# Kernel tuning notes

Measured on AMD Instinct MI355X. Metric: run time of the kernel, lower is better.

The kernel has to match this reference:

```python
import jax, jax.numpy as jnp
import numpy as np

HIDDEN = 4096
N_HEADS = 32
N_KV_HEADS = 8
HEAD_DIM = HIDDEN // N_HEADS  # 128
ROPE_THETA = 10000.0


def rotate_half(x):
    x1, x2 = jnp.split(x, 2, axis=-1)
    return jnp.concatenate((-x2, x1), axis=-1)


def rope_cos_sin(seq_len, dim, theta, dtype):
    inv_freq = 1.0 / (theta ** (jnp.arange(0, dim, 2, dtype=jnp.float32) / dim))
    t = jnp.arange(seq_len, dtype=jnp.float32)
    freqs = jnp.outer(t, inv_freq)               # [S, D/2]
    emb = jnp.concatenate((freqs, freqs), axis=-1)  # [S, D]
    return jnp.cos(emb).astype(dtype), jnp.sin(emb).astype(dtype)


def setup_inputs() -> dict:
    key = jax.random.key(0)
    k0, k1, k2, k3, k4 = jax.random.split(key, 5)
    B, S = 1, 2048
    std = 1.0 / np.sqrt(HIDDEN)
    return {
        "hidden_states": jax.random.normal(k0, (B, S, HIDDEN), dtype=jnp.float32),
        "wq": jax.random.normal(k1, (N_HEADS * HEAD_DIM, HIDDEN), dtype=jnp.float32) * std,
        "wk": jax.random.normal(k2, (N_KV_HEADS * HEAD_DIM, HIDDEN), dtype=jnp.float32) * std,
        "wv": jax.random.normal(k3, (N_KV_HEADS * HEAD_DIM, HIDDEN), dtype=jnp.float32) * std,
        "wo": jax.random.normal(k4, (HIDDEN, N_HEADS * HEAD_DIM), dtype=jnp.float32) * std,
    }


def reference(hidden_states, wq, wk, wv, wo):
    B, S, _ = hidden_states.shape
    dtype = hidden_states.dtype
    G = N_HEADS // N_KV_HEADS  # query groups per kv head

    # projections (torch Linear: x @ W.T)
    q = (hidden_states @ wq.T).reshape(B, S, N_HEADS, HEAD_DIM).transpose(0, 2, 1, 3)      # [B,H,S,D]
    k = (hidden_states @ wk.T).reshape(B, S, N_KV_HEADS, HEAD_DIM).transpose(0, 2, 1, 3)   # [B,Hkv,S,D]
    v = (hidden_states @ wv.T).reshape(B, S, N_KV_HEADS, HEAD_DIM).transpose(0, 2, 1, 3)   # [B,Hkv,S,D]

    cos, sin = rope_cos_sin(S, HEAD_DIM, ROPE_THETA, dtype)  # [S,D]
    cos = cos[None, None]  # [1,1,S,D]
    sin = sin[None, None]
    q = q * cos + rotate_half(q) * sin
    k = k * cos + rotate_half(k) * sin

    # GQA: group query heads with their kv head (equivalent to repeat_interleave on kv)
    qg = q.reshape(B, N_KV_HEADS, G, S, HEAD_DIM)
    scale = 1.0 / np.sqrt(HEAD_DIM)
    scores = jnp.einsum("bkgsd,bktd->bkgst", qg, k) * scale  # [B,Hkv,G,S,S]

    causal = jnp.tril(jnp.ones((S, S), dtype=bool))
    scores = jnp.where(causal, scores, -jnp.inf)
    probs = jax.nn.softmax(scores.astype(jnp.float32), axis=-1).astype(dtype)

    out = jnp.einsum("bkgst,bktd->bkgsd", probs, v)  # [B,Hkv,G,S,D]
    out = out.reshape(B, N_HEADS, S, HEAD_DIM).transpose(0, 2, 1, 3).reshape(B, S, N_HEADS * HEAD_DIM)
    return out @ wo.T
```

## Files before the change

kernel.cpp:

```cpp
#include <hip/hip_runtime.h>
#include <hip/hip_bf16.h>


typedef _Float16 half4_t __attribute__((ext_vector_type(4)));
typedef _Float16 half8_t __attribute__((ext_vector_type(8)));
typedef float f32x4 __attribute__((ext_vector_type(4)));

#define S_LEN 2048
#define HID 4096
#define NH 32
#define NKV 8

__device__ __forceinline__ void gload_lds16(const void* g, void* l) {
  __builtin_amdgcn_global_load_lds((const __attribute__((address_space(1))) void*)g,
                                   (__attribute__((address_space(3))) void*)l, 16, 0, 0);
}

__global__ __launch_bounds__(256) void cvt_f32_f16(const float* __restrict__ src,
                                                   _Float16* __restrict__ dst, int n4) {
  int i = blockIdx.x * 256 + threadIdx.x;
  if (i >= n4) return;
  f32x4 v = *(const f32x4*)(src + (size_t)i * 4);
  half4_t h = {(_Float16)v[0], (_Float16)v[1], (_Float16)v[2], (_Float16)v[3]};
  *(half4_t*)(dst + (size_t)i * 4) = h;
}

__global__ __launch_bounds__(256) void rope_table_kernel(float* __restrict__ cost,
                                                         float* __restrict__ sint) {
  int i = blockIdx.x * 256 + threadIdx.x;
  int d = i & 63;
  int s = i >> 6;
  float inv = exp2f(-(float)d * (13.287712379549449f / 64.0f));
  float f = (float)s * inv;
  cost[i] = cosf(f);
  sint[i] = sinf(f);
}

__global__ __launch_bounds__(256) void rope_apply_q(_Float16* __restrict__ X,
                                                    const float* __restrict__ cost,
                                                    const float* __restrict__ sint) {
  int idx = blockIdx.x * 256 + threadIdx.x;
  int g = idx & 15;
  int tmp = idx >> 4;
  int h = tmp % NH;
  int s = tmp / NH;
  int d0 = g * 4;
  size_t base = (size_t)s * HID + h * 128 + d0;
  half4_t x1 = *(half4_t*)(X + base);
  half4_t x2 = *(half4_t*)(X + base + 64);
  const float* cp = cost + s * 64 + d0;
  const float* sp = sint + s * 64 + d0;
  half4_t y1, y2;
#pragma unroll
  for (int j = 0; j < 4; ++j) {
    float c = cp[j], sn = sp[j];
    float a = (float)x1[j], b = (float)x2[j];
    y1[j] = (_Float16)(a * c - b * sn);
    y2[j] = (_Float16)(b * c + a * sn);
  }
  *(half4_t*)(X + base) = y1;
  *(half4_t*)(X + base + 64) = y2;
}

__global__ __launch_bounds__(256) void rope_k2_inplace(_Float16* __restrict__ K2,
                                                       const float* __restrict__ cost,
                                                       const float* __restrict__ sint) {
  int idx = blockIdx.x * 256 + threadIdx.x;
  int g = idx & 15;
  int tmp = idx >> 4;
  int h = tmp % NKV;
  int s = tmp / NKV;
  int d0 = g * 4;
  size_t tb = (size_t)h * (S_LEN * 128) + (size_t)(s >> 4) * 2048 + (size_t)(s & 15) * 8;
  size_t a1 = tb + (size_t)(d0 >> 3) * 128 + (d0 & 7);
  size_t a2 = a1 + 1024;
  half4_t x1 = *(half4_t*)(K2 + a1);
  half4_t x2 = *(half4_t*)(K2 + a2);
  const float* cp = cost + s * 64 + d0;
  const float* sp = sint + s * 64 + d0;
  half4_t y1, y2;
#pragma unroll
  for (int j = 0; j < 4; ++j) {
    float c = cp[j], sn = sp[j];
    float a = (float)x1[j], b = (float)x2[j];
    y1[j] = (_Float16)(a * c - b * sn);
    y2[j] = (_Float16)(b * c + a * sn);
  }
  *(half4_t*)(K2 + a1) = y1;
  *(half4_t*)(K2 + a2) = y2;
}

template <int MODE>
__global__ __launch_bounds__(256) void gemm5(const _Float16* __restrict__ A,
                                             const _Float16* __restrict__ W0,
                                             const _Float16* __restrict__ W1,
                                             const _Float16* __restrict__ W2,
                                             void* __restrict__ out,
                                             _Float16* __restrict__ K2,
                                             _Float16* __restrict__ V2, int bxoff) {
  __shared__ __align__(16) _Float16 As[2][128 * 32];
  __shared__ __align__(16) _Float16 Bs[2][128 * 32];
  const int t = threadIdx.x, w = t >> 6, l = t & 63, lr = l & 15, lg = l >> 4;
  const int nwg = gridDim.x * gridDim.y;
  const int flat = blockIdx.y * gridDim.x + blockIdx.x;
  const int rm = (flat & 7) * (nwg >> 3) + (flat >> 3);
  const int bx = rm % gridDim.x + bxoff;
  const int by = rm / gridDim.x;
  const int m0 = by * 128;
  const _Float16* Wsel;
  int col0, sel;
  if (MODE == 1) {
    Wsel = W0; col0 = bx * 128; sel = 0;
  } else {
    if (bx < 32)      { Wsel = W0; col0 = bx * 128; sel = 0; }
    else if (bx < 40) { Wsel = W1; col0 = (bx - 32) * 128; sel = 1; }
    else              { Wsel = W2; col0 = (bx - 40) * 128; sel = 2; }
  }
  const int wm = (w >> 1) * 64, wn = (w & 1) * 64;
  const int srow = l >> 2, scol = (l & 3) * 8;
  const _Float16* ap = A + (size_t)m0 * 4096 + scol;
  const _Float16* bp = Wsel + (size_t)col0 * 4096 + scol;
  f32x4 acc[4][4] = {};

#define STAGE5(as_, bs_, kb_)                                     \
  _Pragma("unroll") for (int it = 0; it < 2; ++it) {              \
    const int ci = it * 4 + w;                                    \
    const int r = ci * 16 + srow;                                 \
    gload_lds16(ap + (size_t)r * 4096 + (kb_), (as_) + ci * 512); \
    gload_lds16(bp + (size_t)r * 4096 + (kb_), (bs_) + ci * 512); \
  }

  STAGE5(As[0], Bs[0], 0)
  __syncthreads();
  int cur = 0;
  for (int kb = 0; kb < 4096; kb += 32) {
    if (kb + 32 < 4096) {
      STAGE5(As[cur ^ 1], Bs[cur ^ 1], kb + 32)
    }
    half8_t af[4], bf[4];
#pragma unroll
    for (int mi = 0; mi < 4; ++mi)
      af[mi] = *(const half8_t*)(As[cur] + (wm + mi * 16 + lr) * 32 + lg * 8);
#pragma unroll
    for (int ni = 0; ni < 4; ++ni)
      bf[ni] = *(const half8_t*)(Bs[cur] + (wn + ni * 16 + lr) * 32 + lg * 8);
#pragma unroll
    for (int mi = 0; mi < 4; ++mi)
#pragma unroll
      for (int ni = 0; ni < 4; ++ni)
        acc[mi][ni] = __builtin_amdgcn_mfma_f32_16x16x32_f16(af[mi], bf[ni], acc[mi][ni], 0, 0, 0);
    __syncthreads();
    cur ^= 1;
  }
#undef STAGE5

#pragma unroll
  for (int mi = 0; mi < 4; ++mi) {
#pragma unroll
    for (int ni = 0; ni < 4; ++ni) {
      const int row = m0 + wm + mi * 16 + lg * 4;
      const int col = col0 + wn + ni * 16 + lr;
      if (MODE == 1) {
#pragma unroll
        for (int i = 0; i < 4; ++i)
          ((float*)out)[(size_t)(row + i) * 4096 + col] = acc[mi][ni][i];
      } else if (sel == 0) {
#pragma unroll
        for (int i = 0; i < 4; ++i)
          ((_Float16*)out)[(size_t)(row + i) * 4096 + col] = (_Float16)acc[mi][ni][i];
      } else if (sel == 1) {
        const int h = col >> 7, d = col & 127;
        const size_t kb2 = (size_t)h * (S_LEN * 128) + (size_t)(row >> 4) * 2048 +
                           (size_t)(d >> 3) * 128 + (d & 7);
#pragma unroll
        for (int i = 0; i < 4; ++i)
          K2[kb2 + ((row + i) & 15) * 8] = (_Float16)acc[mi][ni][i];
      } else {
        half4_t o;
#pragma unroll
        for (int i = 0; i < 4; ++i) o[i] = (_Float16)acc[mi][ni][i];
        *(half4_t*)(V2 + (size_t)(col >> 7) * (S_LEN * 128) + (size_t)(row >> 4) * 2048 +
                    (size_t)(col & 127) * 16 + (row & 15)) = o;
      }
    }
  }
}

__global__ __launch_bounds__(256) void attn_kernel(const _Float16* __restrict__ Q,
                                                   const _Float16* __restrict__ K2,
                                                   const _Float16* __restrict__ V2,
                                                   _Float16* __restrict__ Op,
                                                   float* __restrict__ Md) {
  const int bid = blockIdx.x;
  const int hk = bid & 7;
  const int split = (bid >> 3) & 1;
  const int qt = 63 - (bid >> 4);
  const int w = threadIdx.x >> 6;
  const int h = hk * 4 + w;
  const int l = threadIdx.x & 63;
  const int lr = l & 15;
  const int lg = l >> 4;
  const float scale = 0.08838834764831845f;
  const float LOG2E = 1.4426950408889634f;
  const float NEG = -1.0e30f;

  const int half_steps = qt + 1;
  const int kt0 = split * half_steps;
  const int kt1 = kt0 + half_steps;

  int sq[2];
  half8_t qf[2][4];
#pragma unroll
  for (int qc = 0; qc < 2; ++qc) {
    sq[qc] = qt * 32 + qc * 16 + lr;
#pragma unroll
    for (int c = 0; c < 4; ++c)
      qf[qc][c] = *(const half8_t*)(Q + (size_t)sq[qc] * HID + h * 128 + c * 32 + lg * 8);
  }
  const _Float16* Kb = K2 + (size_t)hk * (S_LEN * 128);
  const _Float16* Vb = V2 + (size_t)hk * (S_LEN * 128);

  f32x4 acc[8][2] = {};
  float m[2] = {NEG, NEG};
  float den[2] = {0.f, 0.f};

  for (int kt = kt0; kt < kt1; ++kt) {
    half8_t kf[4];
#pragma unroll
    for (int c = 0; c < 4; ++c)
      kf[c] = *(const half8_t*)(Kb + (size_t)kt * 2048 + (c * 4 + lg) * 128 + lr * 8);
    f32x4 s0 = {0.f, 0.f, 0.f, 0.f}, s1 = {0.f, 0.f, 0.f, 0.f};
#pragma unroll
    for (int c = 0; c < 4; ++c) {
      s0 = __builtin_amdgcn_mfma_f32_16x16x32_f16(kf[c], qf[0][c], s0, 0, 0, 0);
      s1 = __builtin_amdgcn_mfma_f32_16x16x32_f16(kf[c], qf[1][c], s1, 0, 0, 0);
    }
    const int kbase = kt * 16 + lg * 4;
    float sc[2][4];
#pragma unroll
    for (int i = 0; i < 4; ++i) {
      sc[0][i] = s0[i] * scale;
      sc[1][i] = s1[i] * scale;
    }
    if (kt >= 2 * qt) {
#pragma unroll
      for (int qc = 0; qc < 2; ++qc)
#pragma unroll
        for (int i = 0; i < 4; ++i)
          if (kbase + i > sq[qc]) sc[qc][i] = NEG;
    }
    half4_t pf[2];
#pragma unroll
    for (int qc = 0; qc < 2; ++qc) {
      float mx = fmaxf(fmaxf(sc[qc][0], sc[qc][1]), fmaxf(sc[qc][2], sc[qc][3]));
      mx = fmaxf(mx, __shfl_xor(mx, 16));
      mx = fmaxf(mx, __shfl_xor(mx, 32));
      if (!__all(mx - m[qc] <= 8.0f)) {
        float mn = fmaxf(m[qc], mx);
        float corr = exp2f((m[qc] - mn) * LOG2E);
        den[qc] *= corr;
#pragma unroll
        for (int dc = 0; dc < 8; ++dc)
#pragma unroll
          for (int i = 0; i < 4; ++i) acc[dc][qc][i] *= corr;
        m[qc] = mn;
      }
      float ps = 0.f, p[4];
#pragma unroll
      for (int i = 0; i < 4; ++i) {
        p[i] = exp2f((sc[qc][i] - m[qc]) * LOG2E);
        ps += p[i];
      }
      ps += __shfl_xor(ps, 16);
      ps += __shfl_xor(ps, 32);
      den[qc] += ps;
      pf[qc] = (half4_t){(_Float16)p[0], (_Float16)p[1], (_Float16)p[2], (_Float16)p[3]};
    }
#pragma unroll
    for (int dc = 0; dc < 8; ++dc) {
      half4_t vf = *(const half4_t*)(Vb + (size_t)kt * 2048 + (dc * 16 + lr) * 16 + lg * 4);
      acc[dc][0] = __builtin_amdgcn_mfma_f32_16x16x16f16(vf, pf[0], acc[dc][0], 0, 0, 0);
      acc[dc][1] = __builtin_amdgcn_mfma_f32_16x16x16f16(vf, pf[1], acc[dc][1], 0, 0, 0);
    }
  }

  _Float16* Os = Op + (size_t)split * S_LEN * HID;
#pragma unroll
  for (int qc = 0; qc < 2; ++qc) {
    float inv = den[qc] > 0.f ? 1.0f / den[qc] : 0.f;
#pragma unroll
    for (int dc = 0; dc < 8; ++dc) {
      half4_t o;
#pragma unroll
      for (int i = 0; i < 4; ++i) o[i] = (_Float16)(acc[dc][qc][i] * inv);
      *(half4_t*)(Os + (size_t)sq[qc] * HID + h * 128 + dc * 16 + lg * 4) = o;
    }
    if (lg == 0) {
      int mdix = ((split * S_LEN + sq[qc]) * NH + h) * 2;
      Md[mdix] = m[qc];
      Md[mdix + 1] = den[qc];
    }
  }
}

__global__ __launch_bounds__(256) void attn_combine(const _Float16* __restrict__ Op,
                                                    const float* __restrict__ Md,
                                                    _Float16* __restrict__ O) {
  const float LOG2E = 1.4426950408889634f;
  int idx = blockIdx.x * 256 + threadIdx.x;
  int dd = (idx & 15) * 8;
  int h = (idx >> 4) & 31;
  int s = idx >> 9;
  int base = (s * NH + h) * 2;
  float m0 = Md[base], den0 = Md[base + 1];
  float m1 = Md[S_LEN * NH * 2 + base], den1 = Md[S_LEN * NH * 2 + base + 1];
  float M = fmaxf(m0, m1);
  float w0 = den0 * exp2f((m0 - M) * LOG2E);
  float w1 = den1 * exp2f((m1 - M) * LOG2E);
  float r = 1.0f / (w0 + w1);
  w0 *= r;
  w1 *= r;
  size_t off = (size_t)s * HID + h * 128 + dd;
  half8_t a = *(const half8_t*)(Op + off);
  half8_t b = *(const half8_t*)(Op + (size_t)S_LEN * HID + off);
  half8_t o;
#pragma unroll
  for (int j = 0; j < 8; ++j) o[j] = (_Float16)(w0 * (float)a[j] + w1 * (float)b[j]);
  *(half8_t*)(O + off) = o;
}

extern "C" void kernel_launch(void* const* d_in, const int* in_sizes, int n_in,
                              void* d_out, int out_size, void* d_ws, size_t ws_size,
                              hipStream_t stream) {
  (void)in_sizes; (void)n_in; (void)out_size;
  const float* hs = (const float*)d_in[0];
  const float* wq = (const float*)d_in[1];
  const float* wk = (const float*)d_in[2];
  const float* wv = (const float*)d_in[3];
  const float* wo = (const float*)d_in[4];

  char* ws = (char*)d_ws;
  _Float16* hs_h = (_Float16*)(ws);
  _Float16* K2   = (_Float16*)(ws + (32u << 20));
  _Float16* V2   = (_Float16*)(ws + (36u << 20));
  float* cost    = (float*)(ws + (40u << 20));
  float* sint    = (float*)(ws + (40u << 20) + (512u << 10));
  _Float16* q_h  = (_Float16*)(ws + (16u << 20));
  _Float16* wbuf = (_Float16*)(ws + (41u << 20));
  _Float16* Op   = wbuf;
  float* Md      = (float*)(ws + (73u << 20));
  _Float16* o_h  = hs_h;

  cvt_f32_f16<<<8192, 256, 0, stream>>>(hs, hs_h, (S_LEN * HID) / 4);
  rope_table_kernel<<<(S_LEN * 64) / 256, 256, 0, stream>>>(cost, sint);

  const bool merged = ws_size >= (90ull << 20);
  if (merged) {
    _Float16* wk_h = (_Float16*)(ws + (73u << 20));
    _Float16* wv_h = (_Float16*)(ws + (81u << 20));
    cvt_f32_f16<<<16384, 256, 0, stream>>>(wq, wbuf, (HID * HID) / 4);
    cvt_f32_f16<<<4096, 256, 0, stream>>>(wk, wk_h, (NKV * 128 * HID) / 4);
    cvt_f32_f16<<<4096, 256, 0, stream>>>(wv, wv_h, (NKV * 128 * HID) / 4);
    gemm5<0><<<dim3(48, 16), 256, 0, stream>>>(hs_h, wbuf, wk_h, wv_h, q_h, K2, V2, 0);
  } else {
    _Float16* wk_h = wbuf;
    _Float16* wv_h = wbuf + (8u << 20) / 2;
    cvt_f32_f16<<<16384, 256, 0, stream>>>(wq, wbuf, (HID * HID) / 4);
    gemm5<0><<<dim3(32, 16), 256, 0, stream>>>(hs_h, wbuf, nullptr, nullptr, q_h, K2, V2, 0);
    cvt_f32_f16<<<4096, 256, 0, stream>>>(wk, wk_h, (NKV * 128 * HID) / 4);
    cvt_f32_f16<<<4096, 256, 0, stream>>>(wv, wv_h, (NKV * 128 * HID) / 4);
    gemm5<0><<<dim3(16, 16), 256, 0, stream>>>(hs_h, nullptr, wk_h, wv_h, q_h, K2, V2, 32);
  }

  rope_apply_q<<<(S_LEN * NH * 16) / 256, 256, 0, stream>>>(q_h, cost, sint);
  rope_k2_inplace<<<(S_LEN * NKV * 16) / 256, 256, 0, stream>>>(K2, cost, sint);

  attn_kernel<<<1024, 256, 0, stream>>>(q_h, K2, V2, Op, Md);
  attn_combine<<<4096, 256, 0, stream>>>(Op, Md, o_h);

  cvt_f32_f16<<<16384, 256, 0, stream>>>(wo, wbuf, (HID * HID) / 4);
  gemm5<1><<<dim3(32, 16), 256, 0, stream>>>(o_h, wbuf, nullptr, nullptr, d_out, nullptr, nullptr, 0);
}
```

Baseline: 402.1 us.

## Replace GEMM with 256x256 tile ping-pong kernel and fused QKV weight conversion

Introduces a 512-thread GEMM with 256x256 output tiles, K-step 64, XOR-swizzled LDS staging, and interleaved LDS loads and MFMA phases separated by barriers with s_setprio. The Q/K/V weights are converted into one contiguous fp16 buffer by a single kernel, so one GEMM launch covers all three projections. The goal is higher data reuse and MFMA utilisation per CU and fewer launches. The trade-off is much smaller grids (192 and 128 blocks), which may leave CUs idle, and the workspace size check is removed.

```diff
diff --git a/kernel.cpp b/kernel.cpp
--- a/kernel.cpp
+++ b/kernel.cpp
@@ -23,6 +23,23 @@
   f32x4 v = *(const f32x4*)(src + (size_t)i * 4);
   half4_t h = {(_Float16)v[0], (_Float16)v[1], (_Float16)v[2], (_Float16)v[3]};
   *(half4_t*)(dst + (size_t)i * 4) = h;
+}
+
+__global__ __launch_bounds__(256) void cvt_qkv(const float* __restrict__ wq,
+                                               const float* __restrict__ wk,
+                                               const float* __restrict__ wv,
+                                               _Float16* __restrict__ dst, int n4) {
+  int i = blockIdx.x * 256 + threadIdx.x;
+  if (i >= n4) return;
+  size_t e = (size_t)i * 4;
+  const float* src;
+  size_t off;
+  if (e < (size_t)4096 * 4096)      { src = wq; off = e; }
+  else if (e < (size_t)5120 * 4096) { src = wk; off = e - (size_t)4096 * 4096; }
+  else                              { src = wv; off = e - (size_t)5120 * 4096; }
+  f32x4 v = *(const f32x4*)(src + off);
+  half4_t h = {(_Float16)v[0], (_Float16)v[1], (_Float16)v[2], (_Float16)v[3]};
+  *(half4_t*)(dst + e) = h;
 }
 
 __global__ __launch_bounds__(256) void rope_table_kernel(float* __restrict__ cost,
@@ -91,96 +108,147 @@
 }
 
 template <int MODE>
-__global__ __launch_bounds__(256) void gemm5(const _Float16* __restrict__ A,
-                                             const _Float16* __restrict__ W0,
-                                             const _Float16* __restrict__ W1,
-                                             const _Float16* __restrict__ W2,
-                                             void* __restrict__ out,
-                                             _Float16* __restrict__ K2,
-                                             _Float16* __restrict__ V2, int bxoff) {
-  __shared__ __align__(16) _Float16 As[2][128 * 32];
-  __shared__ __align__(16) _Float16 Bs[2][128 * 32];
-  const int t = threadIdx.x, w = t >> 6, l = t & 63, lr = l & 15, lg = l >> 4;
-  const int nwg = gridDim.x * gridDim.y;
-  const int flat = blockIdx.y * gridDim.x + blockIdx.x;
-  const int rm = (flat & 7) * (nwg >> 3) + (flat >> 3);
-  const int bx = rm % gridDim.x + bxoff;
-  const int by = rm / gridDim.x;
-  const int m0 = by * 128;
-  const _Float16* Wsel;
-  int col0, sel;
-  if (MODE == 1) {
-    Wsel = W0; col0 = bx * 128; sel = 0;
-  } else {
-    if (bx < 32)      { Wsel = W0; col0 = bx * 128; sel = 0; }
-    else if (bx < 40) { Wsel = W1; col0 = (bx - 32) * 128; sel = 1; }
-    else              { Wsel = W2; col0 = (bx - 40) * 128; sel = 2; }
-  }
-  const int wm = (w >> 1) * 64, wn = (w & 1) * 64;
-  const int srow = l >> 2, scol = (l & 3) * 8;
-  const _Float16* ap = A + (size_t)m0 * 4096 + scol;
-  const _Float16* bp = Wsel + (size_t)col0 * 4096 + scol;
-  f32x4 acc[4][4] = {};
-
-#define STAGE5(as_, bs_, kb_)                                     \
-  _Pragma("unroll") for (int it = 0; it < 2; ++it) {              \
-    const int ci = it * 4 + w;                                    \
-    const int r = ci * 16 + srow;                                 \
-    gload_lds16(ap + (size_t)r * 4096 + (kb_), (as_) + ci * 512); \
-    gload_lds16(bp + (size_t)r * 4096 + (kb_), (bs_) + ci * 512); \
-  }
-
-  STAGE5(As[0], Bs[0], 0)
-  __syncthreads();
+__global__ __launch_bounds__(512, 2) void gemm8(const _Float16* __restrict__ A,
+                                                const _Float16* __restrict__ W,
+                                                void* __restrict__ out,
+                                                _Float16* __restrict__ K2,
+                                                _Float16* __restrict__ V2) {
+  __shared__ __align__(16) _Float16 As[2][2][128 * 64];
+  __shared__ __align__(16) _Float16 Bs[2][2][128 * 64];
+  const int t = threadIdx.x;
+  const int wid = t >> 6, l = t & 63, lr = l & 15, lg = l >> 4;
+  const int wm = wid >> 2, wn = wid & 3;
+  const int m0 = blockIdx.y * 256, n0 = blockIdx.x * 256;
+  const int NT = 4096 / 64;
+
+  const _Float16* Abase = A + (size_t)m0 * 4096;
+  const _Float16* Wbase = W + (size_t)n0 * 4096;
+
+  f32x4 acc[8][4] = {};
+  half8_t af[4][2], bf[4][2];
+
+#define STAGE_A(buf_, kb_)                                                              \
+  _Pragma("unroll") for (int hh = 0; hh < 2; ++hh)                                      \
+  _Pragma("unroll") for (int j = 0; j < 2; ++j) {                                       \
+    const int ciw = j * 512 + wid * 64;                           \
+    const int ci = ciw + l;                                                             \
+    const int r = ci >> 3, c8 = ci & 7;                                                 \
+    gload_lds16(Abase + (size_t)(hh * 128 + r) * 4096 + (kb_) + ((c8 ^ (r & 7)) << 3),  \
+                &As[buf_][hh][ciw * 8]);                                                \
+  }
+#define STAGE_B(buf_, kb_)                                                              \
+  _Pragma("unroll") for (int hh = 0; hh < 2; ++hh)                                      \
+  _Pragma("unroll") for (int j = 0; j < 2; ++j) {                                       \
+    const int ciw = j * 512 + wid * 64;                                                 \
+    const int ci = ciw + l;                                                             \
+    const int r = ci >> 3, c8 = ci & 7;                                                 \
+    gload_lds16(Wbase + (size_t)(hh * 128 + r) * 4096 + (kb_) + ((c8 ^ (r & 7)) << 3),  \
+                &Bs[buf_][hh][ciw * 8]);                                                \
+  }
+#define LDA(mlo_)                                                                       \
+  _Pragma("unroll") for (int mi = 0; mi < 4; ++mi)                                      \
+  _Pragma("unroll") for (int kk = 0; kk < 2; ++kk) {                                    \
+    const int c8 = (kk * 4 + lg) ^ (lr & 7);                                            \
+    af[mi][kk] = *(const half8_t*)&As[cur][wm][(((mlo_) + mi) * 16 + lr) * 64 + c8 * 8];\
+  }
+#define LDB(nlo_)                                                                       \
+  _Pragma("unroll") for (int ni = 0; ni < 2; ++ni)                                      \
+  _Pragma("unroll") for (int kk = 0; kk < 2; ++kk) {                                    \
+    const int c8 = (kk * 4 + lg) ^ (lr & 7);                                            \
+    bf[(nlo_) + ni][kk] = *(const half8_t*)&Bs[cur][wn >> 1]                            \
+        [((wn & 1) * 64 + ((nlo_) + ni) * 16 + lr) * 64 + c8 * 8];                      \
+  }
+#define MFMA16(mlo_, nlo_)                                                              \
+  _Pragma("unroll") for (int mi = 0; mi < 4; ++mi)                                      \
+  _Pragma("unroll") for (int ni = 0; ni < 2; ++ni)                                      \
+  _Pragma("unroll") for (int kk = 0; kk < 2; ++kk)                                      \
+    acc[(mlo_) + mi][(nlo_) + ni] = __builtin_amdgcn_mfma_f32_16x16x32_f16(             \
+        af[mi][kk], bf[(nlo_) + ni][kk], acc[(mlo_) + mi][(nlo_) + ni], 0, 0, 0);
+
+  STAGE_A(0, 0)
+  STAGE_B(0, 0)
+  asm volatile("s_waitcnt vmcnt(0)" ::: "memory");
+  __builtin_amdgcn_sched_barrier(0);
+  __builtin_amdgcn_s_barrier();
+
   int cur = 0;
-  for (int kb = 0; kb < 4096; kb += 32) {
-    if (kb + 32 < 4096) {
-      STAGE5(As[cur ^ 1], Bs[cur ^ 1], kb + 32)
-    }
-    half8_t af[4], bf[4];
-#pragma unroll
-    for (int mi = 0; mi < 4; ++mi)
-      af[mi] = *(const half8_t*)(As[cur] + (wm + mi * 16 + lr) * 32 + lg * 8);
-#pragma unroll
-    for (int ni = 0; ni < 4; ++ni)
-      bf[ni] = *(const half8_t*)(Bs[cur] + (wn + ni * 16 + lr) * 32 + lg * 8);
-#pragma unroll
-    for (int mi = 0; mi < 4; ++mi)
-#pragma unroll
-      for (int ni = 0; ni < 4; ++ni)
-        acc[mi][ni] = __builtin_amdgcn_mfma_f32_16x16x32_f16(af[mi], bf[ni], acc[mi][ni], 0, 0, 0);
-    __syncthreads();
+  for (int kt = 0; kt < NT; ++kt) {
+    const int nkb = (kt + 1) << 6;
+    const bool pre = (kt + 1 < NT);
+    LDA(0)
+    LDB(0)
+    if (pre) { STAGE_A(cur ^ 1, nkb) }
+    __builtin_amdgcn_sched_barrier(0);
+    __builtin_amdgcn_s_barrier();
+    __builtin_amdgcn_s_setprio(1);
+    MFMA16(0, 0)
+    __builtin_amdgcn_s_setprio(0);
+    __builtin_amdgcn_sched_barrier(0);
+    __builtin_amdgcn_s_barrier();
+    LDB(2)
+    if (pre) { STAGE_B(cur ^ 1, nkb) }
+    __builtin_amdgcn_sched_barrier(0);
+    __builtin_amdgcn_s_barrier();
+    __builtin_amdgcn_s_setprio(1);
+    MFMA16(0, 2)
+    __builtin_amdgcn_s_setprio(0);
+    __builtin_amdgcn_sched_barrier(0);
+    __builtin_amdgcn_s_barrier();
+    LDA(4)
+    __builtin_amdgcn_sched_barrier(0);
+    __builtin_amdgcn_s_barrier();
+    __builtin_amdgcn_s_setprio(1);
+    MFMA16(4, 2)
+    __builtin_amdgcn_s_setprio(0);
+    __builtin_amdgcn_sched_barrier(0);
+    __builtin_amdgcn_s_barrier();
+    __builtin_amdgcn_s_setprio(1);
+    MFMA16(4, 0)
+    __builtin_amdgcn_s_setprio(0);
+    asm volatile("s_waitcnt vmcnt(0)" ::: "memory");
+    __builtin_amdgcn_sched_barrier(0);
+    __builtin_amdgcn_s_barrier();
     cur ^= 1;
   }
-#undef STAGE5
-
-#pragma unroll
-  for (int mi = 0; mi < 4; ++mi) {
+#undef STAGE_A
+#undef STAGE_B
+#undef LDA
+#undef LDB
+#undef MFMA16
+
+  const int grow0 = m0 + wm * 128;
+  const int gcol0 = n0 + wn * 64;
+#pragma unroll
+  for (int mi = 0; mi < 8; ++mi) {
 #pragma unroll
     for (int ni = 0; ni < 4; ++ni) {
-      const int row = m0 + wm + mi * 16 + lg * 4;
-      const int col = col0 + wn + ni * 16 + lr;
+      const int row = grow0 + mi * 16 + lg * 4;
+      const int col = gcol0 + ni * 16 + lr;
       if (MODE == 1) {
 #pragma unroll
         for (int i = 0; i < 4; ++i)
           ((float*)out)[(size_t)(row + i) * 4096 + col] = acc[mi][ni][i];
-      } else if (sel == 0) {
-#pragma unroll
-        for (int i = 0; i < 4; ++i)
-          ((_Float16*)out)[(size_t)(row + i) * 4096 + col] = (_Float16)acc[mi][ni][i];
-      } else if (sel == 1) {
-        const int h = col >> 7, d = col & 127;
-        const size_t kb2 = (size_t)h * (S_LEN * 128) + (size_t)(row >> 4) * 2048 +
-                           (size_t)(d >> 3) * 128 + (d & 7);
-#pragma unroll
-        for (int i = 0; i < 4; ++i)
-          K2[kb2 + ((row + i) & 15) * 8] = (_Float16)acc[mi][ni][i];
       } else {
-        half4_t o;
-#pragma unroll
-        for (int i = 0; i < 4; ++i) o[i] = (_Float16)acc[mi][ni][i];
-        *(half4_t*)(V2 + (size_t)(col >> 7) * (S_LEN * 128) + (size_t)(row >> 4) * 2048 +
-                    (size_t)(col & 127) * 16 + (row & 15)) = o;
+        if (col < 4096) {
+#pragma unroll
+          for (int i = 0; i < 4; ++i)
+            ((_Float16*)out)[(size_t)(row + i) * 4096 + col] = (_Float16)acc[mi][ni][i];
+        } else if (col < 5120) {
+          const int c = col - 4096;
+          const int h = c >> 7, d = c & 127;
+          const size_t kb2 = (size_t)h * (S_LEN * 128) + (size_t)(row >> 4) * 2048 +
+                             (size_t)(d >> 3) * 128 + (d & 7);
+#pragma unroll
+          for (int i = 0; i < 4; ++i)
+            K2[kb2 + ((row + i) & 15) * 8] = (_Float16)acc[mi][ni][i];
+        } else {
+          const int c = col - 5120;
+          half4_t o;
+#pragma unroll
+          for (int i = 0; i < 4; ++i) o[i] = (_Float16)acc[mi][ni][i];
+          *(half4_t*)(V2 + (size_t)(c >> 7) * (S_LEN * 128) + (size_t)(row >> 4) * 2048 +
+                      (size_t)(c & 127) * 16 + (row & 15)) = o;
+        }
       }
     }
   }
@@ -332,7 +400,7 @@
 extern "C" void kernel_launch(void* const* d_in, const int* in_sizes, int n_in,
                               void* d_out, int out_size, void* d_ws, size_t ws_size,
                               hipStream_t stream) {
-  (void)in_sizes; (void)n_in; (void)out_size;
+  (void)in_sizes; (void)n_in; (void)out_size; (void)ws_size;
   const float* hs = (const float*)d_in[0];
   const float* wq = (const float*)d_in[1];
   const float* wk = (const float*)d_in[2];
@@ -341,36 +409,22 @@
 
   char* ws = (char*)d_ws;
   _Float16* hs_h = (_Float16*)(ws);
+  _Float16* q_h  = (_Float16*)(ws + (16u << 20));
   _Float16* K2   = (_Float16*)(ws + (32u << 20));
   _Float16* V2   = (_Float16*)(ws + (36u << 20));
   float* cost    = (float*)(ws + (40u << 20));
   float* sint    = (float*)(ws + (40u << 20) + (512u << 10));
-  _Float16* q_h  = (_Float16*)(ws + (16u << 20));
-  _Float16* wbuf = (_Float16*)(ws + (41u << 20));
-  _Float16* Op   = wbuf;
+  _Float16* wqkv = (_Float16*)(ws + (41u << 20));
+  _Float16* Op   = wqkv;
   float* Md      = (float*)(ws + (73u << 20));
+  _Float16* wo_h = wqkv;
   _Float16* o_h  = hs_h;
 
   cvt_f32_f16<<<8192, 256, 0, stream>>>(hs, hs_h, (S_LEN * HID) / 4);
   rope_table_kernel<<<(S_LEN * 64) / 256, 256, 0, stream>>>(cost, sint);
-
-  const bool merged = ws_size >= (90ull << 20);
-  if (merged) {
-    _Float16* wk_h = (_Float16*)(ws + (73u << 20));
-    _Float16* wv_h = (_Float16*)(ws + (81u << 20));
-    cvt_f32_f16<<<16384, 256, 0, stream>>>(wq, wbuf, (HID * HID) / 4);
-    cvt_f32_f16<<<4096, 256, 0, stream>>>(wk, wk_h, (NKV * 128 * HID) / 4);
-    cvt_f32_f16<<<4096, 256, 0, stream>>>(wv, wv_h, (NKV * 128 * HID) / 4);
-    gemm5<0><<<dim3(48, 16), 256, 0, stream>>>(hs_h, wbuf, wk_h, wv_h, q_h, K2, V2, 0);
-  } else {
-    _Float16* wk_h = wbuf;
-    _Float16* wv_h = wbuf + (8u << 20) / 2;
-    cvt_f32_f16<<<16384, 256, 0, stream>>>(wq, wbuf, (HID * HID) / 4);
-    gemm5<0><<<dim3(32, 16), 256, 0, stream>>>(hs_h, wbuf, nullptr, nullptr, q_h, K2, V2, 0);
-    cvt_f32_f16<<<4096, 256, 0, stream>>>(wk, wk_h, (NKV * 128 * HID) / 4);
-    cvt_f32_f16<<<4096, 256, 0, stream>>>(wv, wv_h, (NKV * 128 * HID) / 4);
-    gemm5<0><<<dim3(16, 16), 256, 0, stream>>>(hs_h, nullptr, wk_h, wv_h, q_h, K2, V2, 32);
-  }
+  cvt_qkv<<<24576, 256, 0, stream>>>(wq, wk, wv, wqkv, (6144 * 4096) / 4);
+
+  gemm8<0><<<dim3(24, 8), 512, 0, stream>>>(hs_h, wqkv, q_h, K2, V2);
 
   rope_apply_q<<<(S_LEN * NH * 16) / 256, 256, 0, stream>>>(q_h, cost, sint);
   rope_k2_inplace<<<(S_LEN * NKV * 16) / 256, 256, 0, stream>>>(K2, cost, sint);
@@ -378,6 +432,6 @@
   attn_kernel<<<1024, 256, 0, stream>>>(q_h, K2, V2, Op, Md);
   attn_combine<<<4096, 256, 0, stream>>>(Op, Md, o_h);
 
-  cvt_f32_f16<<<16384, 256, 0, stream>>>(wo, wbuf, (HID * HID) / 4);
-  gemm5<1><<<dim3(32, 16), 256, 0, stream>>>(o_h, wbuf, nullptr, nullptr, d_out, nullptr, nullptr, 0);
-}
+  cvt_f32_f16<<<16384, 256, 0, stream>>>(wo, wo_h, (HID * HID) / 4);
+  gemm8<1><<<dim3(16, 8), 512, 0, stream>>>(o_h, wo_h, d_out, nullptr, nullptr);
+}
```

Measured after the change: 399.4 us. Within noise of the previous version (-0.7%).

## Fuse fp32-to-fp16 weight conversion into GEMM B-tile loading

Applied to the files above, without the earlier changes.

The GEMM kernels now read fp32 weights straight from global memory into registers, convert them to fp16 and write them into shared memory, replacing the separate weight conversion kernels and their workspace round trips. The B-tile load is software-pipelined two stages ahead through registers, while the A tile still uses direct global-to-LDS loads. The grid swizzle remapping of blocks is also removed. Each block now re-reads fp32 weights, which doubles B traffic per tile and adds conversion ALU and register pressure inside the main loop.

```diff
diff --git a/kernel.cpp b/kernel.cpp
--- a/kernel.cpp
+++ b/kernel.cpp
@@ -91,59 +91,78 @@
 }
 
 template <int MODE>
-__global__ __launch_bounds__(256) void gemm5(const _Float16* __restrict__ A,
-                                             const _Float16* __restrict__ W0,
-                                             const _Float16* __restrict__ W1,
-                                             const _Float16* __restrict__ W2,
+__global__ __launch_bounds__(256) void gemmC(const _Float16* __restrict__ A,
+                                             const float* __restrict__ W0,
+                                             const float* __restrict__ W1,
+                                             const float* __restrict__ W2,
                                              void* __restrict__ out,
                                              _Float16* __restrict__ K2,
-                                             _Float16* __restrict__ V2, int bxoff) {
+                                             _Float16* __restrict__ V2) {
   __shared__ __align__(16) _Float16 As[2][128 * 32];
   __shared__ __align__(16) _Float16 Bs[2][128 * 32];
   const int t = threadIdx.x, w = t >> 6, l = t & 63, lr = l & 15, lg = l >> 4;
-  const int nwg = gridDim.x * gridDim.y;
-  const int flat = blockIdx.y * gridDim.x + blockIdx.x;
-  const int rm = (flat & 7) * (nwg >> 3) + (flat >> 3);
-  const int bx = rm % gridDim.x + bxoff;
-  const int by = rm / gridDim.x;
-  const int m0 = by * 128;
-  const _Float16* Wsel;
+  const int m0 = blockIdx.y * 128;
+  const int bx = blockIdx.x;
+  const float* Wp;
   int col0, sel;
   if (MODE == 1) {
-    Wsel = W0; col0 = bx * 128; sel = 0;
+    Wp = W0; col0 = bx * 128; sel = 0;
   } else {
-    if (bx < 32)      { Wsel = W0; col0 = bx * 128; sel = 0; }
-    else if (bx < 40) { Wsel = W1; col0 = (bx - 32) * 128; sel = 1; }
-    else              { Wsel = W2; col0 = (bx - 40) * 128; sel = 2; }
+    if (bx < 32)      { Wp = W0; col0 = bx * 128; sel = 0; }
+    else if (bx < 40) { Wp = W1; col0 = (bx - 32) * 128; sel = 1; }
+    else              { Wp = W2; col0 = (bx - 40) * 128; sel = 2; }
   }
   const int wm = (w >> 1) * 64, wn = (w & 1) * 64;
-  const int srow = l >> 2, scol = (l & 3) * 8;
-  const _Float16* ap = A + (size_t)m0 * 4096 + scol;
-  const _Float16* bp = Wsel + (size_t)col0 * 4096 + scol;
+  const int srowA = l >> 2, scolA = (l & 3) * 8;
+  const int srowB = t >> 2, scolB = (t & 3) * 8;
+  const _Float16* ap = A + (size_t)m0 * 4096 + scolA;
+  const float* bp = Wp + (size_t)col0 * 4096 + scolB;
+
   f32x4 acc[4][4] = {};
-
-#define STAGE5(as_, bs_, kb_)                                     \
-  _Pragma("unroll") for (int it = 0; it < 2; ++it) {              \
-    const int ci = it * 4 + w;                                    \
-    const int r = ci * 16 + srow;                                 \
-    gload_lds16(ap + (size_t)r * 4096 + (kb_), (as_) + ci * 512); \
-    gload_lds16(bp + (size_t)r * 4096 + (kb_), (bs_) + ci * 512); \
-  }
-
-  STAGE5(As[0], Bs[0], 0)
+  f32x4 br[2][2];
+
+#define GLOAD_A(buf_, kb_)                                            \
+  _Pragma("unroll") for (int it = 0; it < 2; ++it) {                  \
+    const int ci = it * 4 + w;                                        \
+    const int r = ci * 16 + srowA;                                    \
+    gload_lds16(ap + (size_t)r * 4096 + (kb_), &As[buf_][ci * 512]);  \
+  }
+#define LOAD_B(kb_)                                                   \
+  _Pragma("unroll") for (int it = 0; it < 2; ++it) {                  \
+    const float* p = bp + (size_t)(it * 64 + srowB) * 4096 + (kb_);   \
+    br[it][0] = *(const f32x4*)p;                                     \
+    br[it][1] = *(const f32x4*)(p + 4);                               \
+  }
+#define WRITE_B(buf_)                                                 \
+  _Pragma("unroll") for (int it = 0; it < 2; ++it) {                  \
+    half8_t hv;                                                       \
+    _Pragma("unroll") for (int j = 0; j < 4; ++j) {                   \
+      hv[j] = (_Float16)br[it][0][j];                                 \
+      hv[4 + j] = (_Float16)br[it][1][j];                             \
+    }                                                                 \
+    *(half8_t*)&Bs[buf_][(it * 64 + srowB) * 32 + scolB] = hv;        \
+  }
+
+  LOAD_B(0)
+  GLOAD_A(0, 0)
+  WRITE_B(0)
+  LOAD_B(32)
   __syncthreads();
+
   int cur = 0;
   for (int kb = 0; kb < 4096; kb += 32) {
     if (kb + 32 < 4096) {
-      STAGE5(As[cur ^ 1], Bs[cur ^ 1], kb + 32)
+      WRITE_B(cur ^ 1)
+      GLOAD_A(cur ^ 1, kb + 32)
+      if (kb + 64 < 4096) LOAD_B(kb + 64)
     }
     half8_t af[4], bf[4];
 #pragma unroll
     for (int mi = 0; mi < 4; ++mi)
-      af[mi] = *(const half8_t*)(As[cur] + (wm + mi * 16 + lr) * 32 + lg * 8);
+      af[mi] = *(const half8_t*)&As[cur][(wm + mi * 16 + lr) * 32 + lg * 8];
 #pragma unroll
     for (int ni = 0; ni < 4; ++ni)
-      bf[ni] = *(const half8_t*)(Bs[cur] + (wn + ni * 16 + lr) * 32 + lg * 8);
+      bf[ni] = *(const half8_t*)&Bs[cur][(wn + ni * 16 + lr) * 32 + lg * 8];
 #pragma unroll
     for (int mi = 0; mi < 4; ++mi)
 #pragma unroll
@@ -152,7 +171,9 @@
     __syncthreads();
     cur ^= 1;
   }
-#undef STAGE5
+#undef GLOAD_A
+#undef LOAD_B
+#undef WRITE_B
 
 #pragma unroll
   for (int mi = 0; mi < 4; ++mi) {
@@ -332,7 +353,7 @@
 extern "C" void kernel_launch(void* const* d_in, const int* in_sizes, int n_in,
                               void* d_out, int out_size, void* d_ws, size_t ws_size,
                               hipStream_t stream) {
-  (void)in_sizes; (void)n_in; (void)out_size;
+  (void)in_sizes; (void)n_in; (void)out_size; (void)ws_size;
   const float* hs = (const float*)d_in[0];
   const float* wq = (const float*)d_in[1];
   const float* wk = (const float*)d_in[2];
@@ -341,36 +362,19 @@
 
   char* ws = (char*)d_ws;
   _Float16* hs_h = (_Float16*)(ws);
+  _Float16* q_h  = (_Float16*)(ws + (16u << 20));
   _Float16* K2   = (_Float16*)(ws + (32u << 20));
   _Float16* V2   = (_Float16*)(ws + (36u << 20));
   float* cost    = (float*)(ws + (40u << 20));
   float* sint    = (float*)(ws + (40u << 20) + (512u << 10));
-  _Float16* q_h  = (_Float16*)(ws + (16u << 20));
-  _Float16* wbuf = (_Float16*)(ws + (41u << 20));
-  _Float16* Op   = wbuf;
+  _Float16* Op   = (_Float16*)(ws + (41u << 20));
   float* Md      = (float*)(ws + (73u << 20));
   _Float16* o_h  = hs_h;
 
   cvt_f32_f16<<<8192, 256, 0, stream>>>(hs, hs_h, (S_LEN * HID) / 4);
   rope_table_kernel<<<(S_LEN * 64) / 256, 256, 0, stream>>>(cost, sint);
 
-  const bool merged = ws_size >= (90ull << 20);
-  if (merged) {
-    _Float16* wk_h = (_Float16*)(ws + (73u << 20));
-    _Float16* wv_h = (_Float16*)(ws + (81u << 20));
-    cvt_f32_f16<<<16384, 256, 0, stream>>>(wq, wbuf, (HID * HID) / 4);
-    cvt_f32_f16<<<4096, 256, 0, stream>>>(wk, wk_h, (NKV * 128 * HID) / 4);
-    cvt_f32_f16<<<4096, 256, 0, stream>>>(wv, wv_h, (NKV * 128 * HID) / 4);
-    gemm5<0><<<dim3(48, 16), 256, 0, stream>>>(hs_h, wbuf, wk_h, wv_h, q_h, K2, V2, 0);
-  } else {
-    _Float16* wk_h = wbuf;
-    _Float16* wv_h = wbuf + (8u << 20) / 2;
-    cvt_f32_f16<<<16384, 256, 0, stream>>>(wq, wbuf, (HID * HID) / 4);
-    gemm5<0><<<dim3(32, 16), 256, 0, stream>>>(hs_h, wbuf, nullptr, nullptr, q_h, K2, V2, 0);
-    cvt_f32_f16<<<4096, 256, 0, stream>>>(wk, wk_h, (NKV * 128 * HID) / 4);
-    cvt_f32_f16<<<4096, 256, 0, stream>>>(wv, wv_h, (NKV * 128 * HID) / 4);
-    gemm5<0><<<dim3(16, 16), 256, 0, stream>>>(hs_h, nullptr, wk_h, wv_h, q_h, K2, V2, 32);
-  }
+  gemmC<0><<<dim3(48, 16), 256, 0, stream>>>(hs_h, wq, wk, wv, q_h, K2, V2);
 
   rope_apply_q<<<(S_LEN * NH * 16) / 256, 256, 0, stream>>>(q_h, cost, sint);
   rope_k2_inplace<<<(S_LEN * NKV * 16) / 256, 256, 0, stream>>>(K2, cost, sint);
@@ -378,6 +382,5 @@
   attn_kernel<<<1024, 256, 0, stream>>>(q_h, K2, V2, Op, Md);
   attn_combine<<<4096, 256, 0, stream>>>(Op, Md, o_h);
 
-  cvt_f32_f16<<<16384, 256, 0, stream>>>(wo, wbuf, (HID * HID) / 4);
-  gemm5<1><<<dim3(32, 16), 256, 0, stream>>>(o_h, wbuf, nullptr, nullptr, d_out, nullptr, nullptr, 0);
-}
+  gemmC<1><<<dim3(32, 16), 256, 0, stream>>>(o_h, wo, nullptr, nullptr, d_out, nullptr, nullptr);
+}
```

Measured after the change: 393.7 us. -2.1%, faster.
